# Optimization experiments

Measured on AMD Instinct MI355X. Metric: run time of the kernel, lower is better.

## Reference

```python
import jax, jax.numpy as jnp
import numpy as np
from jax import lax

# SoftDTW constants from module-level `sdtw = SoftDTW(use_cuda=False, gamma=0.01, warp=134.4)`
GAMMA = 0.01
WARP = 134.4
BIG = 1e9        # finite stand-in for inf boundary (grad-safe; exp(-BIG/GAMMA) underflows to exactly 0)
MASK_INF = 100000.0
# loss alphas (config.loss.*)
KL_ALPHA = 1.0
KL_FWD_ALPHA = 1.0
GEN_ALPHA = 1.0
GEN_E2E_ALPHA = 1.0
FEAT_ALPHA = 2.0
DUR_ALPHA = 1.0
PITCH_ALPHA = 1.0
MEL_ALPHA = 45.0


def soft_dtw(D):
    """Soft-DTW with warp penalty (NaturalSpeech variant).
    D: [b, n, m] cost matrix. Returns [b] soft-DTW values R[n-1, m-1] of
      R[i,j] = D[i,j] + softmin_gamma(R[i-1,j-1], R[i-1,j]+warp, R[i,j-1]+warp)
    computed over anti-diagonals (wavefront) so each scan step is vectorized.
    """
    b, n, m = D.shape
    K = n + m - 1
    i_idx = jnp.arange(n)
    ks = jnp.arange(K)

    def pack(k):  # pack anti-diagonal k of D, indexed by row i
        j = k - i_idx
        v = (j >= 0) & (j < m)
        return jnp.where(v[None, :], D[:, i_idx, jnp.clip(j, 0, m - 1)], 0.0), v

    Dd, Vd = jax.vmap(pack)(ks)  # Dd: [K, b, n], Vd: [K, n]
    init = jnp.full((b, n), BIG, dtype=D.dtype)

    def step(carry, xs):
        r1, r2 = carry  # previous diag (k-1) and diag (k-2), indexed by row i
        dk, v, k = xs
        # diagonal predecessor (i-1, j-1): on diag k-2 at row i-1; (−1,−1) boundary = 0 only at k==0
        first = jnp.where(k == 0, 0.0, BIG).astype(D.dtype)
        r_diag = jnp.concatenate([jnp.broadcast_to(first, (b, 1)), r2[:, :-1]], axis=1)
        # up predecessor (i-1, j): diag k-1, row i-1
        r_up = jnp.concatenate([jnp.full((b, 1), BIG, dtype=D.dtype), r1[:, :-1]], axis=1)
        # left predecessor (i, j-1): diag k-1, row i
        stacked = jnp.stack([-r_diag, -(r_up + WARP), -(r1 + WARP)]) / GAMMA
        smin = -GAMMA * jax.nn.logsumexp(stacked, axis=0)
        r_new = jnp.where(v[None, :], dk + smin, BIG)
        return (r_new, r1), None

    (rf, _), _ = lax.scan(step, (init, init), (Dd, Vd, ks))
    return rf[:, n - 1]  # cell (n-1, m-1) lies on the last diagonal at row n-1


def kl_matrix(z, lq, m, lp):
    """kl[b,p,q] = sum_h lp - lq - 0.5 + 0.5*(z-m)^2*exp(-2lp); rows (m,lp) [b,h,P], cols (z,lq) [b,h,Q]."""
    h = m.shape[1]
    a = jnp.exp(-2.0 * lp)  # [b,h,P]
    quad = (jnp.einsum('bhp,bhq->bpq', a, z * z)
            - 2.0 * jnp.einsum('bhp,bhq->bpq', a * m, z)
            + jnp.sum(a * m * m, axis=1)[:, :, None])
    return jnp.sum(lp, axis=1)[:, :, None] - jnp.sum(lq, axis=1)[:, None, :] - 0.5 * h + 0.5 * quad


def kl_loss_sdtw(z, lq, m, lp, p_mask, q_mask):
    kl = kl_matrix(z, lq, m, lp)
    kl = jnp.pad(kl, ((0, 0), (0, 1), (0, 1)))
    pmf = jnp.pad(p_mask.astype(jnp.float32), ((0, 0), (0, 1)))
    qmf = jnp.pad(q_mask.astype(jnp.float32), ((0, 0), (0, 1)))
    pb, qb = pmf.astype(bool), qmf.astype(bool)
    kl = jnp.where(pb[:, :, None] ^ qb[:, None, :], MASK_INF, kl)
    kl = jnp.where((~pb[:, :, None]) & (~qb[:, None, :]), 0.0, kl)
    return soft_dtw(kl).sum() / pmf.sum()


def setup_inputs() -> dict:
    key = jax.random.key(0)
    ks = jax.random.split(key, 16)
    B, H, T = 8, 192, 400
    d = {
        'mel_slice': jax.random.normal(ks[0], (B, 80, T), jnp.float32),
        'mel_slice_hat': jax.random.normal(ks[1], (B, 80, T), jnp.float32),
        'scores_disc_fake': jax.random.normal(ks[2], (6, B, T), jnp.float32),
        'scores_disc_fake_e2e': jax.random.normal(ks[3], (6, B, T), jnp.float32),
        'feats_disc_real': jax.random.normal(ks[4], (30, B, 128, T), jnp.float32),
        'feats_disc_fake': jax.random.normal(ks[5], (30, B, 128, T), jnp.float32),
        'duration_loss': jax.random.uniform(ks[6], (1,), jnp.float32),
        'pitch_loss': jax.random.uniform(ks[7], (1,), jnp.float32),
        'z_p': jax.random.normal(ks[8], (B, H, T), jnp.float32),
        'm_p': jax.random.normal(ks[9], (B, H, T), jnp.float32),
        'logs_p': jax.random.normal(ks[10], (B, H, T), jnp.float32),
        'z_q': jax.random.normal(ks[11], (B, H, T), jnp.float32),
        'm_q': jax.random.normal(ks[12], (B, H, T), jnp.float32),
        'logs_q': jax.random.normal(ks[13], (B, H, T), jnp.float32),
        'p_mask': jnp.ones((B, T), jnp.int32),
        'z_mask': jnp.ones((B, T), jnp.int32),
    }
    return d


def reference(mel_slice, mel_slice_hat, scores_disc_fake, scores_disc_fake_e2e,
              feats_disc_real, feats_disc_fake, duration_loss, pitch_loss,
              z_p, m_p, logs_p, z_q, m_q, logs_q, p_mask, z_mask):
    # generator losses: sum over discriminator maps of mean((1 - s)^2)
    loss_gen = jnp.mean((1.0 - scores_disc_fake) ** 2, axis=(1, 2)).sum() * GEN_ALPHA
    loss_gen_e2e = jnp.mean((1.0 - scores_disc_fake_e2e) ** 2, axis=(1, 2)).sum() * GEN_E2E_ALPHA
    # feature matching: 2 * sum over feature maps of mean|real.detach() - fake|
    fr = lax.stop_gradient(feats_disc_real)
    loss_fm = 2.0 * jnp.mean(jnp.abs(fr - feats_disc_fake), axis=(1, 2, 3)).sum() * FEAT_ALPHA
    loss_mel = jnp.mean(jnp.abs(mel_slice - mel_slice_hat)) * MEL_ALPHA
    loss_dur = jnp.sum(duration_loss) * DUR_ALPHA
    loss_pitch = jnp.sum(pitch_loss) * PITCH_ALPHA
    # soft-DTW KL (both directions)
    loss_kl = kl_loss_sdtw(z_p, logs_q, m_p, logs_p, p_mask, z_mask) * KL_ALPHA
    loss_kl_fwd = kl_loss_sdtw(z_q, logs_p, m_q, logs_q, z_mask, p_mask) * KL_FWD_ALPHA
    total = loss_gen + loss_gen_e2e + loss_fm + loss_mel + loss_dur + loss_pitch + loss_kl + loss_kl_fwd
    return jnp.stack([loss_gen, loss_gen_e2e, loss_fm, loss_mel, loss_dur,
                      loss_pitch, loss_kl, loss_kl_fwd, total])
```

## Files before the change

### kernel.cpp

```cpp
#include <hip/hip_runtime.h>
#include <math.h>

#define BIGV      1e9f
#define WARP_PEN  134.4f
#define MASK_INF_C 100000.0f

#define B   8
#define H   192
#define T   400
#define NP  401
#define NPROB 16
#define TSLAB 166464
#define SBLOCKS 768
#define KLBLOCKS (49 * NPROB)

typedef float f32x4 __attribute__((ext_vector_type(4)));

#define SLOT_OFF 16
#define LSP_OFF 160
#define LSQ_OFF (160 + B*T)
#define C1P_OFF (160 + 2*B*T)
#define C1Q_OFF (160 + 3*B*T)
#define DMAT_OFF (160 + 4*B*T)

__device__ __forceinline__ int diag_len(int s) { return (s <= 50) ? s + 1 : 101 - s; }
__device__ __forceinline__ int diag_i0 (int s) { return (s <= 50) ? 0 : s - 50; }
__device__ __forceinline__ int diag_Cs (int s) {
    return (s <= 51) ? s * (s + 1) / 2 : 2601 - (101 - s) * (102 - s) / 2;
}

__device__ __forceinline__ float wave_shr1(float src, float fill) {
    int r = __builtin_amdgcn_update_dpp(__float_as_int(fill), __float_as_int(src),
                                        0x138 , 0xf, 0xf, false);
    return __int_as_float(r);
}

__global__ __launch_bounds__(256)
void colsum(const float* __restrict__ logs_p, const float* __restrict__ m_p,
            const float* __restrict__ logs_q, const float* __restrict__ m_q,
            float* __restrict__ ws) {
    int b = blockIdx.x / 7;
    int lane = threadIdx.x & 63;
    int hq = threadIdx.x >> 6;
    int t = (blockIdx.x % 7) * 64 + lane;
    __shared__ float part[4][4][64];
    float lp_s = 0.f, lq_s = 0.f, c1p = 0.f, c1q = 0.f;
    if (t < T) {
        int base = b*H*T + hq*48*T + t;
        const float* LP = logs_p + base;
        const float* MP = m_p   + base;
        const float* LQ = logs_q + base;
        const float* MQ = m_q   + base;
#pragma unroll 4
        for (int h = 0; h < 48; ++h) {
            float lp = LP[h*T], mp = MP[h*T];
            float lq = LQ[h*T], mq = MQ[h*T];
            lp_s += lp;
            lq_s += lq;
            c1p += __expf(-2.f*lp) * mp * mp;
            c1q += __expf(-2.f*lq) * mq * mq;
        }
    }
    part[hq][0][lane] = lp_s;
    part[hq][1][lane] = lq_s;
    part[hq][2][lane] = c1p;
    part[hq][3][lane] = c1q;
    __syncthreads();
    if (hq == 0 && t < T) {
        float a0 = part[0][0][lane] + part[1][0][lane] + part[2][0][lane] + part[3][0][lane];
        float a1 = part[0][1][lane] + part[1][1][lane] + part[2][1][lane] + part[3][1][lane];
        float a2 = part[0][2][lane] + part[1][2][lane] + part[2][2][lane] + part[3][2][lane];
        float a3 = part[0][3][lane] + part[1][3][lane] + part[2][3][lane] + part[3][3][lane];
        ws[LSP_OFF + b*T + t] = a0;
        ws[LSQ_OFF + b*T + t] = a1;
        ws[C1P_OFF + b*T + t] = a2;
        ws[C1Q_OFF + b*T + t] = a3;
    }
}

#define TILE 64
#define KH 16
__global__ __launch_bounds__(256)
void fused_kl_scalar(const float* __restrict__ z_p, const float* __restrict__ m_p,
                     const float* __restrict__ logs_p,
                     const float* __restrict__ z_q, const float* __restrict__ m_q,
                     const float* __restrict__ logs_q,
                     const int* __restrict__ p_mask, const int* __restrict__ z_mask,
                     float* __restrict__ ws,
                     const float* __restrict__ mel, const float* __restrict__ melh,
                     const float* __restrict__ sg,  const float* __restrict__ se,
                     const float* __restrict__ fr,  const float* __restrict__ ff) {
    __shared__ __align__(16) float As [KH][TILE+4];
    __shared__ __align__(16) float AMs[KH][TILE+4];
    __shared__ __align__(16) float Zs [KH][TILE+4];
    __shared__ __align__(16) float Z2s[KH][TILE+4];
    __shared__ float red[4][8];

    if (blockIdx.x < KLBLOCKS) {
        int prob = blockIdx.x / 49;
        int bx   = blockIdx.x % 49;
        int dir = prob >> 3, b = prob & 7;
        int tp = bx / 7, tq = bx % 7;
        int p0 = tp * TILE, q0 = tq * TILE;

        const float* lp_arr = dir ? logs_q : logs_p;
        const float* m_arr  = dir ? m_q    : m_p;
        const float* z_arr  = dir ? z_q    : z_p;
        const float* Lp = ws + (dir ? LSQ_OFF : LSP_OFF) + b*T;
        const float* Lq = ws + (dir ? LSP_OFF : LSQ_OFF) + b*T;
        const float* C1 = ws + (dir ? C1Q_OFF : C1P_OFF) + b*T;
        const int* rmask = dir ? z_mask : p_mask;
        const int* cmask = dir ? p_mask : z_mask;

        int tid = threadIdx.x;
        int tx = tid & 15, ty = tid >> 4;

        float acc1[4][4] = {{0.f}}, acc2[4][4] = {{0.f}};

        const float* lpB = lp_arr + b*H*T;
        const float* mB  = m_arr  + b*H*T;
        const float* zB  = z_arr  + b*H*T;

        for (int h0 = 0; h0 < H; h0 += KH) {
            for (int e = tid; e < KH*TILE; e += 256) {
                int hh = e >> 6, tt = e & 63;
                int pg = p0 + tt; if (pg > T-1) pg = T-1;
                int qg = q0 + tt; if (qg > T-1) qg = T-1;
                float lp = lpB[(h0+hh)*T + pg];
                float mv = mB [(h0+hh)*T + pg];
                float a  = __expf(-2.f*lp);
                As [hh][tt] = a;
                AMs[hh][tt] = a * mv;
                float zv = zB[(h0+hh)*T + qg];
                Zs [hh][tt] = zv;
                Z2s[hh][tt] = zv * zv;
            }
            __syncthreads();
#pragma unroll 8
            for (int hh = 0; hh < KH; ++hh) {
                const float4 av  = *(const float4*)(&As [hh][ty*4]);
                const float4 amv = *(const float4*)(&AMs[hh][ty*4]);
                const float4 zv  = *(const float4*)(&Zs [hh][tx*4]);
                const float4 z2v = *(const float4*)(&Z2s[hh][tx*4]);
                const float pa[4]  = {av.x, av.y, av.z, av.w};
                const float pam[4] = {amv.x, amv.y, amv.z, amv.w};
                const float qz[4]  = {zv.x, zv.y, zv.z, zv.w};
                const float qz2[4] = {z2v.x, z2v.y, z2v.z, z2v.w};
#pragma unroll
                for (int ii = 0; ii < 4; ++ii)
#pragma unroll
                    for (int jj = 0; jj < 4; ++jj) {
                        acc1[ii][jj] = fmaf(pa[ii],  qz2[jj], acc1[ii][jj]);
                        acc2[ii][jj] = fmaf(pam[ii], qz[jj],  acc2[ii][jj]);
                    }
            }
            __syncthreads();
        }

        float* Dm = ws + DMAT_OFF + (size_t)prob * TSLAB;
#pragma unroll
        for (int ii = 0; ii < 4; ++ii) {
            int p = p0 + ty*4 + ii;
            if (p > NP-1) continue;
            int pc = p < T ? p : T-1;
            float lpv = Lp[pc];
            float c1v = C1[pc];
            bool pmv = (p < T) && (rmask[b*T + p] != 0);
#pragma unroll
            for (int jj = 0; jj < 4; ++jj) {
                int q = q0 + tx*4 + jj;
                if (q > NP-1) continue;
                int qc = q < T ? q : T-1;
                bool qmv = (q < T) && (cmask[b*T + q] != 0);
                float val = lpv - Lq[qc] - 0.5f*(float)H
                          + 0.5f*(acc1[ii][jj] - 2.f*acc2[ii][jj] + c1v);
                float outv = (pmv != qmv) ? MASK_INF_C : ((!pmv && !qmv) ? 0.f : val);
                int I8 = p >> 3, J8 = q >> 3, sdg = I8 + J8;
                int len = diag_len(sdg), i0 = diag_i0(sdg), Cs = diag_Cs(sdg);
                int k = (p & 7) * 2 + ((q & 7) >> 2);
                int off = Cs*64 + (k*len + (I8 - i0))*4 + (q & 3);
                Dm[off] = outv;
            }
        }
    } else {
        float s0 = 0.f, s1 = 0.f, s2 = 0.f, s3 = 0.f, s4 = 0.f, s5 = 0.f;
        int tid = (blockIdx.x - KLBLOCKS) * 256 + threadIdx.x;
        const int stride = SBLOCKS * 256;

        const float4* fr4 = (const float4*)fr;
        const float4* ff4 = (const float4*)ff;
        for (int i = tid; i < 3072000; i += stride) {
            float4 a = fr4[i], b = ff4[i];
            s2 += fabsf(a.x - b.x) + fabsf(a.y - b.y) + fabsf(a.z - b.z) + fabsf(a.w - b.w);
        }
        const float4* m4 = (const float4*)mel;
        const float4* mh4 = (const float4*)melh;
        for (int i = tid; i < 64000; i += stride) {
            float4 a = m4[i], b = mh4[i];
            s3 += fabsf(a.x - b.x) + fabsf(a.y - b.y) + fabsf(a.z - b.z) + fabsf(a.w - b.w);
        }
        const float4* g4 = (const float4*)sg;
        const float4* e4 = (const float4*)se;
        for (int i = tid; i < 4800; i += stride) {
            float4 a = g4[i], b = e4[i];
            float gx = 1.f - a.x, gy = 1.f - a.y, gz = 1.f - a.z, gw = 1.f - a.w;
            s0 += gx*gx + gy*gy + gz*gz + gw*gw;
            float hx = 1.f - b.x, hy = 1.f - b.y, hz = 1.f - b.z, hw = 1.f - b.w;
            s1 += hx*hx + hy*hy + hz*hz + hw*hw;
        }
        for (int i = tid; i < B*T; i += stride) {
            s4 += (float)p_mask[i];
            s5 += (float)z_mask[i];
        }
        for (int off = 32; off > 0; off >>= 1) {
            s0 += __shfl_down(s0, off); s1 += __shfl_down(s1, off);
            s2 += __shfl_down(s2, off); s3 += __shfl_down(s3, off);
            s4 += __shfl_down(s4, off); s5 += __shfl_down(s5, off);
        }
        int wid = threadIdx.x >> 6;
        if ((threadIdx.x & 63) == 0) {
            red[wid][0] = s0; red[wid][1] = s1; red[wid][2] = s2;
            red[wid][3] = s3; red[wid][4] = s4; red[wid][5] = s5;
        }
        __syncthreads();
        if (threadIdx.x == 0) {
            float t0 = 0.f, t1 = 0.f, t2 = 0.f, t3 = 0.f, t4 = 0.f, t5 = 0.f;
#pragma unroll
            for (int w = 0; w < 4; ++w) {
                t0 += red[w][0]; t1 += red[w][1]; t2 += red[w][2];
                t3 += red[w][3]; t4 += red[w][4]; t5 += red[w][5];
            }
            float* slot = ws + SLOT_OFF + (blockIdx.x & 7) * 16;
            atomicAdd(&slot[0], t0); atomicAdd(&slot[1], t1);
            atomicAdd(&slot[2], t2); atomicAdd(&slot[3], t3);
            atomicAdd(&slot[4], t4); atomicAdd(&slot[5], t5);
        }
    }
}

__global__ __launch_bounds__(64, 1)
void dtw_diag(const float* __restrict__ Dd, float* __restrict__ acc) {
    int prob = blockIdx.x;
    int lane = threadIdx.x;
    const float* Dp = Dd + (size_t)prob * TSLAB;

    float brow[8], browW[8], rightraw[8], rightW[8];
    float brold = BIGV, v00 = BIGV;
#pragma unroll
    for (int t = 0; t < 8; ++t) {
        brow[t] = BIGV; browW[t] = BIGV; rightraw[t] = BIGV; rightW[t] = BIGV;
    }

    f32x4 bufA[16], bufB[16];

    auto load_diag = [&](int sp, f32x4* buf) {
        if (sp > 100) sp = 100;
        int len = diag_len(sp), i0 = diag_i0(sp), Cs = diag_Cs(sp);
        int pos = lane - i0;
        pos = pos < 0 ? 0 : pos;
        pos = pos > len - 1 ? len - 1 : pos;
        const float* srcb = Dp + Cs*64 + pos*4;
        int str = len * 4;
#pragma unroll
        for (int k = 0; k < 16; ++k)
            buf[k] = *(const f32x4*)(srcb + k*str);
    };

#define TILE_STEP(CUR, NXT, SVAL, DO_LOAD)                                    \
    {                                                                          \
        const int s_ = (SVAL);                                                 \
        if (DO_LOAD) {                                                         \
            load_diag(s_ + 1, NXT);                                            \
            __builtin_amdgcn_sched_barrier(0);  \
        }                                                                      \
        bool jz = (s_ == lane);                                    \
        float brnew = brow[7];                                                 \
        _Pragma("unroll")                                                      \
        for (int c = 0; c < 8; ++c) {                                          \
            brow[c] = wave_shr1(brow[c], BIGV);                                \
            browW[c] = brow[c] + WARP_PEN;                                     \
        }                                                                      \
        float corner = wave_shr1(brold, BIGV);                                 \
        if (jz) corner = (lane == 0) ? 0.f : BIGV;                             \
        float dprev = corner;                                                  \
        _Pragma("unroll")                                                      \
        for (int r = 0; r < 8; ++r) {                                          \
            float leftW = jz ? BIGV : rightW[r];                               \
            float dnextrow = jz ? BIGV : rightraw[r];                          \
            float diag = dprev;                                                \
            _Pragma("unroll")                                                  \
            for (int ch = 0; ch < 2; ++ch) {                                   \
                f32x4 dvv = CUR[r*2 + ch];                                     \
                _Pragma("unroll")                                              \
                for (int cc = 0; cc < 4; ++cc) {                               \
                    const int c = ch*4 + cc;                                   \
                    float v = fminf(fminf(diag, browW[c]), leftW) + dvv[cc];   \
                    if (r == 0 && c == 0) v00 = v;                             \
                    float t_ = brow[c];                                        \
                    brow[c] = v;                                               \
                    float vW = v + WARP_PEN;                                   \
                    browW[c] = vW;                                             \
                    leftW = vW;                                                \
                    diag = t_;                                                 \
                }                                                              \
            }                                                                  \
            rightraw[r] = brow[7];                                             \
            rightW[r]   = browW[7];                                            \
            dprev = dnextrow;                                                  \
        }                                                                      \
        brold = brnew;                                                         \
    }

    load_diag(0, bufA);

    for (int sb = 0; sb < 100; sb += 2) {
        TILE_STEP(bufA, bufB, sb,     1)
        TILE_STEP(bufB, bufA, sb + 1, 1)
    }
    TILE_STEP(bufA, bufB, 100, 0)
#undef TILE_STEP

    if (lane == 50) atomicAdd(&acc[6 + (prob >> 3)], v00);
}

__global__ void finalize(const float* __restrict__ acc,
                         const float* __restrict__ dur,
                         const float* __restrict__ pit,
                         float* __restrict__ out) {
    if (threadIdx.x != 0 || blockIdx.x != 0) return;
    float t[6] = {0.f, 0.f, 0.f, 0.f, 0.f, 0.f};
    for (int s = 0; s < 8; ++s)
        for (int c = 0; c < 6; ++c)
            t[c] += acc[SLOT_OFF + s*16 + c];
    float gen  = t[0] / 3200.f;
    float e2e  = t[1] / 3200.f;
    float fm   = 4.f * t[2] / 409600.f;
    float melv = 45.f * t[3] / 256000.f;
    float d    = dur[0];
    float p    = pit[0];
    float kl   = acc[6] / t[4];
    float klf  = acc[7] / t[5];
    out[0] = gen; out[1] = e2e; out[2] = fm; out[3] = melv;
    out[4] = d;   out[5] = p;   out[6] = kl; out[7] = klf;
    out[8] = gen + e2e + fm + melv + d + p + kl + klf;
}

extern "C" void kernel_launch(void* const* d_in, const int* in_sizes, int n_in,
                              void* d_out, int out_size, void* d_ws, size_t ws_size,
                              hipStream_t stream) {
    const float* mel    = (const float*)d_in[0];
    const float* melh   = (const float*)d_in[1];
    const float* sg     = (const float*)d_in[2];
    const float* se     = (const float*)d_in[3];
    const float* fr     = (const float*)d_in[4];
    const float* ff     = (const float*)d_in[5];
    const float* dur    = (const float*)d_in[6];
    const float* pit    = (const float*)d_in[7];
    const float* z_p    = (const float*)d_in[8];
    const float* m_p    = (const float*)d_in[9];
    const float* logs_p = (const float*)d_in[10];
    const float* z_q    = (const float*)d_in[11];
    const float* m_q    = (const float*)d_in[12];
    const float* logs_q = (const float*)d_in[13];
    const int*   p_mask = (const int*)d_in[14];
    const int*   z_mask = (const int*)d_in[15];
    float* ws  = (float*)d_ws;
    float* out = (float*)d_out;

    hipMemsetAsync(ws, 0, 160 * sizeof(float), stream);
    colsum<<<B*7, 256, 0, stream>>>(logs_p, m_p, logs_q, m_q, ws);
    fused_kl_scalar<<<KLBLOCKS + SBLOCKS, 256, 0, stream>>>(
        z_p, m_p, logs_p, z_q, m_q, logs_q, p_mask, z_mask, ws,
        mel, melh, sg, se, fr, ff);
    dtw_diag<<<NPROB, 64, 0, stream>>>(ws + DMAT_OFF, ws);
    finalize<<<1, 64, 0, stream>>>(ws, dur, pit, out);
}
```

Before: 156.1 us.

## Enlarge KL tile to 128 and reorder DTW tile recurrence into wavefronts

The KL cost-matrix kernel now uses 128x128 tiles with a 2x2 register micro-tile per thread, cutting block count from 49 to 16 per problem. It also drops the Z^2 shared array and squares z in registers instead. Inside each DTW 8x8 tile, the serial row-by-row min-plus recurrence is reordered into 15 anti-diagonals to expose instruction-level parallelism. The costs are more registers (128 accumulators per thread) and fewer KL blocks to overlap with the reduction blocks.

```diff
diff --git a/kernel.cpp b/kernel.cpp
--- a/kernel.cpp
+++ b/kernel.cpp
@@ -12,7 +12,7 @@
 #define NPROB 16
 #define TSLAB 166464
 #define SBLOCKS 768
-#define KLBLOCKS (49 * NPROB)
+#define KL2BLOCKS (16 * NPROB)
 
 typedef float f32x4 __attribute__((ext_vector_type(4)));
 
@@ -78,7 +78,7 @@
     }
 }
 
-#define TILE 64
+#define TILE 128
 #define KH 16
 __global__ __launch_bounds__(256)
 void fused_kl_scalar(const float* __restrict__ z_p, const float* __restrict__ m_p,
@@ -93,14 +93,13 @@
     __shared__ __align__(16) float As [KH][TILE+4];
     __shared__ __align__(16) float AMs[KH][TILE+4];
     __shared__ __align__(16) float Zs [KH][TILE+4];
-    __shared__ __align__(16) float Z2s[KH][TILE+4];
     __shared__ float red[4][8];
 
-    if (blockIdx.x < KLBLOCKS) {
-        int prob = blockIdx.x / 49;
-        int bx   = blockIdx.x % 49;
+    if (blockIdx.x < KL2BLOCKS) {
+        int prob = blockIdx.x >> 4;
+        int tix  = blockIdx.x & 15;
         int dir = prob >> 3, b = prob & 7;
-        int tp = bx / 7, tq = bx % 7;
+        int tp = tix >> 2, tq = tix & 3;
         int p0 = tp * TILE, q0 = tq * TILE;
 
         const float* lp_arr = dir ? logs_q : logs_p;
@@ -115,7 +114,7 @@
         int tid = threadIdx.x;
         int tx = tid & 15, ty = tid >> 4;
 
-        float acc1[4][4] = {{0.f}}, acc2[4][4] = {{0.f}};
+        float acc1[2][2][4][4] = {{{{0.f}}}}, acc2[2][2][4][4] = {{{{0.f}}}};
 
         const float* lpB = lp_arr + b*H*T;
         const float* mB  = m_arr  + b*H*T;
@@ -123,7 +122,7 @@
 
         for (int h0 = 0; h0 < H; h0 += KH) {
             for (int e = tid; e < KH*TILE; e += 256) {
-                int hh = e >> 6, tt = e & 63;
+                int hh = e >> 7, tt = e & 127;
                 int pg = p0 + tt; if (pg > T-1) pg = T-1;
                 int qg = q0 + tt; if (qg > T-1) qg = T-1;
                 float lp = lpB[(h0+hh)*T + pg];
@@ -131,27 +130,38 @@
                 float a  = __expf(-2.f*lp);
                 As [hh][tt] = a;
                 AMs[hh][tt] = a * mv;
-                float zv = zB[(h0+hh)*T + qg];
-                Zs [hh][tt] = zv;
-                Z2s[hh][tt] = zv * zv;
+                Zs [hh][tt] = zB[(h0+hh)*T + qg];
             }
             __syncthreads();
-#pragma unroll 8
+#pragma unroll 4
             for (int hh = 0; hh < KH; ++hh) {
-                const float4 av  = *(const float4*)(&As [hh][ty*4]);
-                const float4 amv = *(const float4*)(&AMs[hh][ty*4]);
-                const float4 zv  = *(const float4*)(&Zs [hh][tx*4]);
-                const float4 z2v = *(const float4*)(&Z2s[hh][tx*4]);
-                const float pa[4]  = {av.x, av.y, av.z, av.w};
-                const float pam[4] = {amv.x, amv.y, amv.z, amv.w};
-                const float qz[4]  = {zv.x, zv.y, zv.z, zv.w};
-                const float qz2[4] = {z2v.x, z2v.y, z2v.z, z2v.w};
+                const float4 aLo  = *(const float4*)(&As [hh][ty*4]);
+                const float4 aHi  = *(const float4*)(&As [hh][64 + ty*4]);
+                const float4 amLo = *(const float4*)(&AMs[hh][ty*4]);
+                const float4 amHi = *(const float4*)(&AMs[hh][64 + ty*4]);
+                const float4 zLo  = *(const float4*)(&Zs [hh][tx*4]);
+                const float4 zHi  = *(const float4*)(&Zs [hh][64 + tx*4]);
+                const float aL[4]  = {aLo.x, aLo.y, aLo.z, aLo.w};
+                const float aH[4]  = {aHi.x, aHi.y, aHi.z, aHi.w};
+                const float amL[4] = {amLo.x, amLo.y, amLo.z, amLo.w};
+                const float amH[4] = {amHi.x, amHi.y, amHi.z, amHi.w};
+                const float zL[4]  = {zLo.x, zLo.y, zLo.z, zLo.w};
+                const float zH[4]  = {zHi.x, zHi.y, zHi.z, zHi.w};
+                float z2L[4], z2H[4];
+#pragma unroll
+                for (int j = 0; j < 4; ++j) { z2L[j] = zL[j]*zL[j]; z2H[j] = zH[j]*zH[j]; }
 #pragma unroll
                 for (int ii = 0; ii < 4; ++ii)
 #pragma unroll
                     for (int jj = 0; jj < 4; ++jj) {
-                        acc1[ii][jj] = fmaf(pa[ii],  qz2[jj], acc1[ii][jj]);
-                        acc2[ii][jj] = fmaf(pam[ii], qz[jj],  acc2[ii][jj]);
+                        acc1[0][0][ii][jj] = fmaf(aL[ii],  z2L[jj], acc1[0][0][ii][jj]);
+                        acc1[0][1][ii][jj] = fmaf(aL[ii],  z2H[jj], acc1[0][1][ii][jj]);
+                        acc1[1][0][ii][jj] = fmaf(aH[ii],  z2L[jj], acc1[1][0][ii][jj]);
+                        acc1[1][1][ii][jj] = fmaf(aH[ii],  z2H[jj], acc1[1][1][ii][jj]);
+                        acc2[0][0][ii][jj] = fmaf(amL[ii], zL[jj],  acc2[0][0][ii][jj]);
+                        acc2[0][1][ii][jj] = fmaf(amL[ii], zH[jj],  acc2[0][1][ii][jj]);
+                        acc2[1][0][ii][jj] = fmaf(amH[ii], zL[jj],  acc2[1][0][ii][jj]);
+                        acc2[1][1][ii][jj] = fmaf(amH[ii], zH[jj],  acc2[1][1][ii][jj]);
                     }
             }
             __syncthreads();
@@ -159,21 +169,25 @@
 
         float* Dm = ws + DMAT_OFF + (size_t)prob * TSLAB;
 #pragma unroll
+        for (int up = 0; up < 2; ++up)
+#pragma unroll
         for (int ii = 0; ii < 4; ++ii) {
-            int p = p0 + ty*4 + ii;
+            int p = p0 + up*64 + ty*4 + ii;
             if (p > NP-1) continue;
             int pc = p < T ? p : T-1;
             float lpv = Lp[pc];
             float c1v = C1[pc];
             bool pmv = (p < T) && (rmask[b*T + p] != 0);
 #pragma unroll
+            for (int uq = 0; uq < 2; ++uq)
+#pragma unroll
             for (int jj = 0; jj < 4; ++jj) {
-                int q = q0 + tx*4 + jj;
+                int q = q0 + uq*64 + tx*4 + jj;
                 if (q > NP-1) continue;
                 int qc = q < T ? q : T-1;
                 bool qmv = (q < T) && (cmask[b*T + q] != 0);
                 float val = lpv - Lq[qc] - 0.5f*(float)H
-                          + 0.5f*(acc1[ii][jj] - 2.f*acc2[ii][jj] + c1v);
+                          + 0.5f*(acc1[up][uq][ii][jj] - 2.f*acc2[up][uq][ii][jj] + c1v);
                 float outv = (pmv != qmv) ? MASK_INF_C : ((!pmv && !qmv) ? 0.f : val);
                 int I8 = p >> 3, J8 = q >> 3, sdg = I8 + J8;
                 int len = diag_len(sdg), i0 = diag_i0(sdg), Cs = diag_Cs(sdg);
@@ -184,7 +198,7 @@
         }
     } else {
         float s0 = 0.f, s1 = 0.f, s2 = 0.f, s3 = 0.f, s4 = 0.f, s5 = 0.f;
-        int tid = (blockIdx.x - KLBLOCKS) * 256 + threadIdx.x;
+        int tid = (blockIdx.x - KL2BLOCKS) * 256 + threadIdx.x;
         const int stride = SBLOCKS * 256;
 
         const float4* fr4 = (const float4*)fr;
@@ -244,12 +258,11 @@
     int lane = threadIdx.x;
     const float* Dp = Dd + (size_t)prob * TSLAB;
 
-    float brow[8], browW[8], rightraw[8], rightW[8];
+    float brow[8];
+    float rightraw[8], rightW[8];
     float brold = BIGV, v00 = BIGV;
 #pragma unroll
-    for (int t = 0; t < 8; ++t) {
-        brow[t] = BIGV; browW[t] = BIGV; rightraw[t] = BIGV; rightW[t] = BIGV;
-    }
+    for (int t = 0; t < 8; ++t) { brow[t] = BIGV; rightraw[t] = BIGV; rightW[t] = BIGV; }
 
     f32x4 bufA[16], bufB[16];
 
@@ -271,43 +284,42 @@
         const int s_ = (SVAL);                                                 \
         if (DO_LOAD) {                                                         \
             load_diag(s_ + 1, NXT);                                            \
-            __builtin_amdgcn_sched_barrier(0);  \
+            __builtin_amdgcn_sched_barrier(0);                                 \
         }                                                                      \
         bool jz = (s_ == lane);                                    \
         float brnew = brow[7];                                                 \
+        float upraw[8], upW[8];                                                \
         _Pragma("unroll")                                                      \
         for (int c = 0; c < 8; ++c) {                                          \
-            brow[c] = wave_shr1(brow[c], BIGV);                                \
-            browW[c] = brow[c] + WARP_PEN;                                     \
+            upraw[c] = wave_shr1(brow[c], BIGV);                               \
+            upW[c] = upraw[c] + WARP_PEN;                                      \
         }                                                                      \
         float corner = wave_shr1(brold, BIGV);                                 \
         if (jz) corner = (lane == 0) ? 0.f : BIGV;                             \
-        float dprev = corner;                                                  \
+        float vr[8][8], vw[8][8];                                              \
         _Pragma("unroll")                                                      \
-        for (int r = 0; r < 8; ++r) {                                          \
-            float leftW = jz ? BIGV : rightW[r];                               \
-            float dnextrow = jz ? BIGV : rightraw[r];                          \
-            float diag = dprev;                                                \
+        for (int d = 0; d < 15; ++d) {                                         \
             _Pragma("unroll")                                                  \
-            for (int ch = 0; ch < 2; ++ch) {                                   \
-                f32x4 dvv = CUR[r*2 + ch];                                     \
-                _Pragma("unroll")                                              \
-                for (int cc = 0; cc < 4; ++cc) {                               \
-                    const int c = ch*4 + cc;                                   \
-                    float v = fminf(fminf(diag, browW[c]), leftW) + dvv[cc];   \
-                    if (r == 0 && c == 0) v00 = v;                             \
-                    float t_ = brow[c];                                        \
-                    brow[c] = v;                                               \
-                    float vW = v + WARP_PEN;                                   \
-                    browW[c] = vW;                                             \
-                    leftW = vW;                                                \
-                    diag = t_;                                                 \
-                }                                                              \
+            for (int r = 0; r < 8; ++r) {                                      \
+                const int c = d - r;                                           \
+                if (c < 0 || c > 7) continue;                                  \
+                float uw = (r == 0) ? upW[c] : vw[r-1][c];                     \
+                float lw = (c == 0) ? (jz ? BIGV : rightW[r]) : vw[r][c-1];    \
+                float dg;                                                      \
+                if (r == 0 && c == 0)      dg = corner;                        \
+                else if (r == 0)           dg = upraw[c-1];                    \
+                else if (c == 0)           dg = jz ? BIGV : rightraw[r-1];     \
+                else                       dg = vr[r-1][c-1];                  \
+                float v = fminf(fminf(uw, lw), dg) + CUR[r*2 + (c>>2)][c&3];   \
+                vr[r][c] = v;                                                  \
+                vw[r][c] = v + WARP_PEN;                                       \
             }                                                                  \
-            rightraw[r] = brow[7];                                             \
-            rightW[r]   = browW[7];                                            \
-            dprev = dnextrow;                                                  \
         }                                                                      \
+        v00 = vr[0][0];                                                        \
+        _Pragma("unroll")                                                      \
+        for (int r = 0; r < 8; ++r) { rightraw[r] = vr[r][7]; rightW[r] = vw[r][7]; } \
+        _Pragma("unroll")                                                      \
+        for (int c = 0; c < 8; ++c) brow[c] = vr[7][c];                        \
         brold = brnew;                                                         \
     }
 
@@ -369,7 +381,7 @@
 
     hipMemsetAsync(ws, 0, 160 * sizeof(float), stream);
     colsum<<<B*7, 256, 0, stream>>>(logs_p, m_p, logs_q, m_q, ws);
-    fused_kl_scalar<<<KLBLOCKS + SBLOCKS, 256, 0, stream>>>(
+    fused_kl_scalar<<<KL2BLOCKS + SBLOCKS, 256, 0, stream>>>(
         z_p, m_p, logs_p, z_q, m_q, logs_q, p_mask, z_mask, ws,
         mel, melh, sg, se, fr, ff);
     dtw_diag<<<NPROB, 64, 0, stream>>>(ws + DMAT_OFF, ws);
```

Result: slower. 180.1 us (+15.4%).
